# Kernel tuning notes

Hardware: AMD Instinct MI355X
Metric: run time of the kernel (lower is better)

## Reference

```python
import jax, jax.numpy as jnp
import numpy as np

N = 8192      # num voxels (queries)
M = 8192      # num important conv coords (keys)
B = 2         # batch size
MAXZ, MAXY, MAXX = 41, 1440, 1440
PTS, PDIM = 5, 4
PRUNE_RATIO = 0.5
NEG = -1e9


def setup_inputs() -> dict:
    key = jax.random.key(0)
    k = jax.random.split(key, 8)
    bidx = jax.random.randint(k[0], (N, 1), 0, B)
    zyx = jnp.concatenate([
        jax.random.randint(k[1], (N, 1), 0, MAXZ),
        jax.random.randint(k[2], (N, 1), 0, MAXY),
        jax.random.randint(k[3], (N, 1), 0, MAXX)], axis=1)
    voxel_coords = jnp.concatenate([bidx, zyx], axis=1).astype(jnp.int32)  # [N,4] (b,z,y,x)
    kb = jax.random.randint(k[4], (M, 1), 0, B).astype(jnp.float32)
    kc = jax.random.uniform(k[5], (M, 3), dtype=jnp.float32) * jnp.array([MAXZ, MAXY, MAXX], jnp.float32)
    important_conv_coords = jnp.concatenate([kb, kc], axis=1)  # [M,4] float
    voxels = jax.random.normal(k[6], (N, PTS, PDIM), dtype=jnp.float32)
    kw = jax.random.split(k[7], 2)
    w1 = jax.random.normal(kw[0], (3, 32), dtype=jnp.float32) * 0.5
    b1 = jnp.zeros((32,), jnp.float32)
    w2 = jax.random.normal(kw[1], (32, 1), dtype=jnp.float32) * 0.2
    b2 = jnp.zeros((1,), jnp.float32)
    return {"voxel_coords": voxel_coords, "important_conv_coords": important_conv_coords,
            "voxels": voxels, "w1": w1, "b1": b1, "w2": w2, "b2": b2}


def reference(voxel_coords, important_conv_coords, voxels, w1, b1, w2, b2):
    # --- attn_prune_unimportant: per-batch coord attention, vectorized with a batch mask ---
    q = voxel_coords[:, 1:].astype(jnp.float32)           # [N,3]
    qb = voxel_coords[:, 0]                               # [N] batch idx
    keys = important_conv_coords[:, 1:]                   # [M,3]
    kbat = important_conv_coords[:, 0].astype(jnp.int32)  # [M]
    scores = jnp.einsum('nd,md->nm', q, keys) / jnp.sqrt(jnp.float32(3.0))  # [N,M]
    mask = qb[:, None] == kbat[None, :]
    scores = jnp.where(mask, scores, NEG)
    attn = jax.nn.softmax(scores, axis=-1)                # per-batch softmax (masked)
    coords_weight = jnp.einsum('nm,md->nd', attn, keys)   # [N,3]  (values == keys)
    # importance_conv: Linear(3,32) -> ReLU -> Linear(32,1) -> Sigmoid
    h = jax.nn.relu(coords_weight @ w1 + b1)
    importance = jax.nn.sigmoid(h @ w2 + b2)              # [N,1]
    # --- sort-based pruning: drop the lowest-importance fraction ---
    order = jnp.argsort(importance[:, 0])                 # ascending, like torch .sort()
    keep = order[int(N * PRUNE_RATIO):]                   # [K] static size
    important_coords = voxel_coords[keep]                 # [K,4]
    important_voxels = voxels[keep]                       # [K,PTS,PDIM]
    kept_importance = importance[keep]                    # [K,1]
    return important_coords, important_voxels, kept_importance, importance
```

## Files before the change

kernel.cpp:

```cpp
#include <hip/hip_runtime.h>
#include <math.h>

#define NQ   8192
#define MK   8192
#define KEEP 4096

#define OFF_CMAX   0
#define OFF_PART   262144
#define OFF_K64    1310720


typedef unsigned long long ull;

__global__ __launch_bounds__(1024) void attn_kernel(
    const int4*   __restrict__ vcoords,
    const float4* __restrict__ kcoords,
    float* __restrict__ ws)
{
    __shared__ __align__(16) char smem[65792];
    float4* sk   = (float4*)smem;
    float*  red1 = (float*)(smem + 16384);
    float*  red2 = (float*)(smem + 16384 + 16448);
    float4* pf   = (float4*)smem;

    float*  cmaxg = (float*)((char*)ws + OFF_CMAX);
    float4* partg = (float4*)((char*)ws + OFF_PART);

    const int b = blockIdx.x;
    const int g = b >> 3, c = b & 7;
    const int gs = g * 256, cs = c * 1024;
    const int t = threadIdx.x, w = t >> 6, lane = t & 63;

    const int4 v0 = vcoords[gs + lane];
    const int4 v1 = vcoords[gs + lane + 64];
    const int4 v2 = vcoords[gs + lane + 128];
    const int4 v3 = vcoords[gs + lane + 192];
    const float qb0 = (float)v0.x, qz0 = (float)v0.y, qy0 = (float)v0.z, qx0 = (float)v0.w;
    const float qb1 = (float)v1.x, qz1 = (float)v1.y, qy1 = (float)v1.z, qx1 = (float)v1.w;
    const float qb2 = (float)v2.x, qz2 = (float)v2.y, qy2 = (float)v2.z, qx2 = (float)v2.w;
    const float qb3 = (float)v3.x, qz3 = (float)v3.y, qy3 = (float)v3.z, qx3 = (float)v3.w;
    const float is3 = 0.57735026918962576f;

    if (t < 1024) sk[t] = kcoords[cs + t];
    __syncthreads();

    const int jb = w * 64, je = jb + 64;

    float m0 = -INFINITY, m1 = -INFINITY, m2 = -INFINITY, m3 = -INFINITY;
    #pragma unroll 4
    for (int j = jb; j < je; ++j) {
        float4 k4 = sk[j];
        float d0 = fmaf(qz0, k4.y, fmaf(qy0, k4.z, qx0 * k4.w));
        float d1 = fmaf(qz1, k4.y, fmaf(qy1, k4.z, qx1 * k4.w));
        float d2 = fmaf(qz2, k4.y, fmaf(qy2, k4.z, qx2 * k4.w));
        float d3 = fmaf(qz3, k4.y, fmaf(qy3, k4.z, qx3 * k4.w));
        m0 = fmaxf(m0, fmaf(fabsf(k4.x - qb0), -1e10f, d0));
        m1 = fmaxf(m1, fmaf(fabsf(k4.x - qb1), -1e10f, d1));
        m2 = fmaxf(m2, fmaf(fabsf(k4.x - qb2), -1e10f, d2));
        m3 = fmaxf(m3, fmaf(fabsf(k4.x - qb3), -1e10f, d3));
    }
    red1[w * 257 + lane]       = m0;
    red1[w * 257 + lane + 64]  = m1;
    red1[w * 257 + lane + 128] = m2;
    red1[w * 257 + lane + 192] = m3;
    __syncthreads();
    {
        const int col = t >> 2, r4 = (t & 3) * 4;
        float mv = red1[r4 * 257 + col];
        mv = fmaxf(mv, red1[(r4 + 1) * 257 + col]);
        mv = fmaxf(mv, red1[(r4 + 2) * 257 + col]);
        mv = fmaxf(mv, red1[(r4 + 3) * 257 + col]);
        mv = fmaxf(mv, __shfl_xor(mv, 1));
        mv = fmaxf(mv, __shfl_xor(mv, 2));
        if ((t & 3) == 0) {
            red2[col] = mv;
            cmaxg[b * 256 + col] = mv;
        }
    }
    __syncthreads();
    const float mg0 = red2[lane],       cut0 = mg0 - 155.8845727f;
    const float mg1 = red2[lane + 64],  cut1 = mg1 - 155.8845727f;
    const float mg2 = red2[lane + 128], cut2 = mg2 - 155.8845727f;
    const float mg3 = red2[lane + 192], cut3 = mg3 - 155.8845727f;

    float l0 = 0.f, sz0 = 0.f, sy0 = 0.f, sx0 = 0.f;
    float l1 = 0.f, sz1 = 0.f, sy1 = 0.f, sx1 = 0.f;
    float l2 = 0.f, sz2 = 0.f, sy2 = 0.f, sx2 = 0.f;
    float l3 = 0.f, sz3 = 0.f, sy3 = 0.f, sx3 = 0.f;
    #pragma unroll 2
    for (int j = jb; j < je; ++j) {
        float4 k4 = sk[j];
        float d0 = fmaf(qz0, k4.y, fmaf(qy0, k4.z, qx0 * k4.w));
        float d1 = fmaf(qz1, k4.y, fmaf(qy1, k4.z, qx1 * k4.w));
        float d2 = fmaf(qz2, k4.y, fmaf(qy2, k4.z, qx2 * k4.w));
        float d3 = fmaf(qz3, k4.y, fmaf(qy3, k4.z, qx3 * k4.w));
        d0 = fmaf(fabsf(k4.x - qb0), -1e10f, d0);
        d1 = fmaf(fabsf(k4.x - qb1), -1e10f, d1);
        d2 = fmaf(fabsf(k4.x - qb2), -1e10f, d2);
        d3 = fmaf(fabsf(k4.x - qb3), -1e10f, d3);
        bool t0 = d0 >= cut0, t1 = d1 >= cut1, t2 = d2 >= cut2, t3 = d3 >= cut3;
        if (__any(t0 || t1 || t2 || t3)) {
            float e0 = t0 ? expf((d0 - mg0) * is3) : 0.f;
            float e1 = t1 ? expf((d1 - mg1) * is3) : 0.f;
            float e2 = t2 ? expf((d2 - mg2) * is3) : 0.f;
            float e3 = t3 ? expf((d3 - mg3) * is3) : 0.f;
            l0 += e0; sz0 = fmaf(e0, k4.y, sz0); sy0 = fmaf(e0, k4.z, sy0); sx0 = fmaf(e0, k4.w, sx0);
            l1 += e1; sz1 = fmaf(e1, k4.y, sz1); sy1 = fmaf(e1, k4.z, sy1); sx1 = fmaf(e1, k4.w, sx1);
            l2 += e2; sz2 = fmaf(e2, k4.y, sz2); sy2 = fmaf(e2, k4.z, sy2); sx2 = fmaf(e2, k4.w, sx2);
            l3 += e3; sz3 = fmaf(e3, k4.y, sz3); sy3 = fmaf(e3, k4.z, sy3); sx3 = fmaf(e3, k4.w, sx3);
        }
    }
    __syncthreads();
    pf[w * 257 + lane]       = make_float4(l0, sz0, sy0, sx0);
    pf[w * 257 + lane + 64]  = make_float4(l1, sz1, sy1, sx1);
    pf[w * 257 + lane + 128] = make_float4(l2, sz2, sy2, sx2);
    pf[w * 257 + lane + 192] = make_float4(l3, sz3, sy3, sx3);
    __syncthreads();
    {
        const int col = t >> 2, r4 = (t & 3) * 4;
        float4 a = pf[r4 * 257 + col];
        #pragma unroll
        for (int rr = 1; rr < 4; ++rr) {
            float4 p = pf[(r4 + rr) * 257 + col];
            a.x += p.x; a.y += p.y; a.z += p.z; a.w += p.w;
        }
        a.x += __shfl_xor(a.x, 1); a.y += __shfl_xor(a.y, 1);
        a.z += __shfl_xor(a.z, 1); a.w += __shfl_xor(a.w, 1);
        a.x += __shfl_xor(a.x, 2); a.y += __shfl_xor(a.y, 2);
        a.z += __shfl_xor(a.z, 2); a.w += __shfl_xor(a.w, 2);
        if ((t & 3) == 0) partg[b * 256 + col] = a;
    }
}

__global__ __launch_bounds__(256) void mlp_kernel(
    const float* __restrict__ ws,
    const float* __restrict__ w1, const float* __restrict__ b1,
    const float* __restrict__ w2, const float* __restrict__ b2,
    float* __restrict__ out_imp, ull* __restrict__ K64)
{
    const int s = blockIdx.x * 256 + threadIdx.x;
    const int g = s >> 8, q = s & 255;
    const float*  cmaxg = (const float*)((const char*)ws + OFF_CMAX);
    const float4* partg = (const float4*)((const char*)ws + OFF_PART);
    const float is3 = 0.57735026918962576f;

    float cc[8];
    float C = -INFINITY;
    #pragma unroll
    for (int c = 0; c < 8; ++c) {
        cc[c] = cmaxg[(g * 8 + c) * 256 + q];
        C = fmaxf(C, cc[c]);
    }
    float L = 0.f, SZ = 0.f, SY = 0.f, SX = 0.f;
    #pragma unroll
    for (int c = 0; c < 8; ++c) {
        float sc = expf((cc[c] - C) * is3);
        float4 p = partg[(g * 8 + c) * 256 + q];
        L  = fmaf(p.x, sc, L);
        SZ = fmaf(p.y, sc, SZ);
        SY = fmaf(p.z, sc, SY);
        SX = fmaf(p.w, sc, SX);
    }
    float inv = (L > 0.f) ? 1.f / L : 0.f;
    float cz = SZ * inv, cy = SY * inv, cx = SX * inv;
    float logit = b2[0];
    #pragma unroll
    for (int k = 0; k < 32; ++k) {
        float h = b1[k] + cz * w1[k] + cy * w1[32 + k] + cx * w1[64 + k];
        h = fmaxf(h, 0.f);
        logit += h * w2[k];
    }
    float p = 1.f / (1.f + expf(-logit));
    out_imp[s] = p;
    K64[s] = ((ull)__float_as_uint(p) << 32) | (unsigned)s;
}

__global__ __launch_bounds__(1024) void rank_scatter_kernel(
    const ull* __restrict__ K,
    const int4* __restrict__ vcoords,
    const float* __restrict__ voxels,
    float* __restrict__ out)
{
    __shared__ int scnt[16][32];
    __shared__ int rks[32];
    const int t = threadIdx.x, w = t >> 6, lane = t & 63;
    const int ib = blockIdx.x * 32;

    const ull kiv = K[ib + (lane & 31)];
    const int kilo = (int)(unsigned)kiv, kihi = (int)(unsigned)(kiv >> 32);

    const int jb = w * 512;
    ull kj[8];
    #pragma unroll
    for (int r = 0; r < 8; ++r) kj[r] = K[jb + r * 64 + lane];

    int acc = 0;
    for (int i = 0; i < 32; ++i) {
        unsigned lo = (unsigned)__builtin_amdgcn_readlane(kilo, i);
        unsigned hi = (unsigned)__builtin_amdgcn_readlane(kihi, i);
        ull ki = ((ull)hi << 32) | lo;
        int c = 0;
        #pragma unroll
        for (int r = 0; r < 8; ++r)
            c += (int)__popcll(__ballot(kj[r] < ki));
        acc += (lane == i) ? c : 0;
    }
    if (lane < 32) scnt[w][lane] = acc;
    __syncthreads();
    if (t < 32) {
        int rank = 0;
        #pragma unroll
        for (int ww = 0; ww < 16; ++ww) rank += scnt[ww][t];
        rks[t] = rank;
    }
    __syncthreads();

    const int il = t >> 5, r = t & 31;
    const int rank = rks[il];
    if (rank >= KEEP) {
        const int p = rank - KEEP;
        const int i = ib + il;
        if (r < 20) {
            out[16384 + p * 20 + r] = voxels[i * 20 + r];
        } else if (r < 24) {
            const int* vc = (const int*)&vcoords[i];
            out[p * 4 + (r - 20)] = (float)vc[r - 20];
        } else if (r == 24) {
            out[98304 + p] = __uint_as_float((unsigned)(K[i] >> 32));
        }
    }
}

extern "C" void kernel_launch(void* const* d_in, const int* in_sizes, int n_in,
                              void* d_out, int out_size, void* d_ws, size_t ws_size,
                              hipStream_t stream) {
    const int4*   vcoords = (const int4*)d_in[0];
    const float4* kcoords = (const float4*)d_in[1];
    const float*  voxels  = (const float*)d_in[2];
    const float*  w1      = (const float*)d_in[3];
    const float*  b1      = (const float*)d_in[4];
    const float*  w2      = (const float*)d_in[5];
    const float*  b2      = (const float*)d_in[6];
    float* out = (float*)d_out;
    float* ws  = (float*)d_ws;
    ull* K64   = (ull*)((char*)d_ws + OFF_K64);

    attn_kernel<<<256, 1024, 0, stream>>>(vcoords, kcoords, ws);
    mlp_kernel<<<32, 256, 0, stream>>>(ws, w1, b1, w2, b2, out + 102400, K64);
    rank_scatter_kernel<<<256, 1024, 0, stream>>>(K64, vcoords, voxels, out);
}
```

Before: 104.4 us.

## Partition keys by batch in shared memory and split attention loops per batch

Keys loaded into shared memory are compacted with a ballot/popcount prefix so batch-0 keys come first and batch-1 keys follow. Each wave then runs separate loops over the batch-0 and batch-1 key ranges, so the per-key batch mask arithmetic (fabs/fma penalty) is dropped and queries choose the matching max or cutoff. Queries still evaluate both ranges but only accumulate for their own batch, and a guard is added in the combine step for chunks with no matching keys (max of -inf). This assumes batch ids are only 0 or 1, and it adds a block sync plus some loop-splitting overhead.

```diff
diff --git a/kernel.cpp b/kernel.cpp
--- a/kernel.cpp
+++ b/kernel.cpp
@@ -21,6 +21,7 @@
     float4* sk   = (float4*)smem;
     float*  red1 = (float*)(smem + 16384);
     float*  red2 = (float*)(smem + 16384 + 16448);
+    int*    wc   = (int*)(smem + 33856);
     float4* pf   = (float4*)smem;
 
     float*  cmaxg = (float*)((char*)ws + OFF_CMAX);
@@ -35,34 +36,54 @@
     const int4 v1 = vcoords[gs + lane + 64];
     const int4 v2 = vcoords[gs + lane + 128];
     const int4 v3 = vcoords[gs + lane + 192];
-    const float qb0 = (float)v0.x, qz0 = (float)v0.y, qy0 = (float)v0.z, qx0 = (float)v0.w;
-    const float qb1 = (float)v1.x, qz1 = (float)v1.y, qy1 = (float)v1.z, qx1 = (float)v1.w;
-    const float qb2 = (float)v2.x, qz2 = (float)v2.y, qy2 = (float)v2.z, qx2 = (float)v2.w;
-    const float qb3 = (float)v3.x, qz3 = (float)v3.y, qy3 = (float)v3.z, qx3 = (float)v3.w;
+    const float qz0 = (float)v0.y, qy0 = (float)v0.z, qx0 = (float)v0.w;
+    const float qz1 = (float)v1.y, qy1 = (float)v1.z, qx1 = (float)v1.w;
+    const float qz2 = (float)v2.y, qy2 = (float)v2.z, qx2 = (float)v2.w;
+    const float qz3 = (float)v3.y, qy3 = (float)v3.z, qx3 = (float)v3.w;
+    const bool qb0 = (v0.x != 0), qb1 = (v1.x != 0);
+    const bool qb2 = (v2.x != 0), qb3 = (v3.x != 0);
     const float is3 = 0.57735026918962576f;
 
-    if (t < 1024) sk[t] = kcoords[cs + t];
+    float4 k4s = kcoords[cs + t];
+    ull bal = __ballot(k4s.x == 0.0f);
+    if (lane == 0) wc[w] = (int)__popcll(bal);
+    __syncthreads();
+    int woff = 0, n0 = 0;
+    #pragma unroll
+    for (int i = 0; i < 16; ++i) { int cv = wc[i]; n0 += cv; if (i < w) woff += cv; }
+    {
+        int bef = (int)__popcll(bal & ((1ull << lane) - 1));
+        int dst = (k4s.x == 0.0f) ? (woff + bef) : (n0 + t - woff - bef);
+        sk[dst] = k4s;
+    }
     __syncthreads();
 
     const int jb = w * 64, je = jb + 64;
-
-    float m0 = -INFINITY, m1 = -INFINITY, m2 = -INFINITY, m3 = -INFINITY;
+    const int jeA = min(je, n0);
+    const int jbB = max(jb, n0);
+
+    float mA0 = -INFINITY, mA1 = -INFINITY, mA2 = -INFINITY, mA3 = -INFINITY;
+    float mB0 = -INFINITY, mB1 = -INFINITY, mB2 = -INFINITY, mB3 = -INFINITY;
     #pragma unroll 4
-    for (int j = jb; j < je; ++j) {
-        float4 k4 = sk[j];
-        float d0 = fmaf(qz0, k4.y, fmaf(qy0, k4.z, qx0 * k4.w));
-        float d1 = fmaf(qz1, k4.y, fmaf(qy1, k4.z, qx1 * k4.w));
-        float d2 = fmaf(qz2, k4.y, fmaf(qy2, k4.z, qx2 * k4.w));
-        float d3 = fmaf(qz3, k4.y, fmaf(qy3, k4.z, qx3 * k4.w));
-        m0 = fmaxf(m0, fmaf(fabsf(k4.x - qb0), -1e10f, d0));
-        m1 = fmaxf(m1, fmaf(fabsf(k4.x - qb1), -1e10f, d1));
-        m2 = fmaxf(m2, fmaf(fabsf(k4.x - qb2), -1e10f, d2));
-        m3 = fmaxf(m3, fmaf(fabsf(k4.x - qb3), -1e10f, d3));
-    }
-    red1[w * 257 + lane]       = m0;
-    red1[w * 257 + lane + 64]  = m1;
-    red1[w * 257 + lane + 128] = m2;
-    red1[w * 257 + lane + 192] = m3;
+    for (int j = jb; j < jeA; ++j) {
+        float4 k4 = sk[j];
+        mA0 = fmaxf(mA0, fmaf(qz0, k4.y, fmaf(qy0, k4.z, qx0 * k4.w)));
+        mA1 = fmaxf(mA1, fmaf(qz1, k4.y, fmaf(qy1, k4.z, qx1 * k4.w)));
+        mA2 = fmaxf(mA2, fmaf(qz2, k4.y, fmaf(qy2, k4.z, qx2 * k4.w)));
+        mA3 = fmaxf(mA3, fmaf(qz3, k4.y, fmaf(qy3, k4.z, qx3 * k4.w)));
+    }
+    #pragma unroll 4
+    for (int j = jbB; j < je; ++j) {
+        float4 k4 = sk[j];
+        mB0 = fmaxf(mB0, fmaf(qz0, k4.y, fmaf(qy0, k4.z, qx0 * k4.w)));
+        mB1 = fmaxf(mB1, fmaf(qz1, k4.y, fmaf(qy1, k4.z, qx1 * k4.w)));
+        mB2 = fmaxf(mB2, fmaf(qz2, k4.y, fmaf(qy2, k4.z, qx2 * k4.w)));
+        mB3 = fmaxf(mB3, fmaf(qz3, k4.y, fmaf(qy3, k4.z, qx3 * k4.w)));
+    }
+    red1[w * 257 + lane]       = qb0 ? mB0 : mA0;
+    red1[w * 257 + lane + 64]  = qb1 ? mB1 : mA1;
+    red1[w * 257 + lane + 128] = qb2 ? mB2 : mA2;
+    red1[w * 257 + lane + 192] = qb3 ? mB3 : mA3;
     __syncthreads();
     {
         const int col = t >> 2, r4 = (t & 3) * 4;
@@ -82,23 +103,42 @@
     const float mg1 = red2[lane + 64],  cut1 = mg1 - 155.8845727f;
     const float mg2 = red2[lane + 128], cut2 = mg2 - 155.8845727f;
     const float mg3 = red2[lane + 192], cut3 = mg3 - 155.8845727f;
+    const float cA0 = qb0 ? INFINITY : cut0, cB0 = qb0 ? cut0 : INFINITY;
+    const float cA1 = qb1 ? INFINITY : cut1, cB1 = qb1 ? cut1 : INFINITY;
+    const float cA2 = qb2 ? INFINITY : cut2, cB2 = qb2 ? cut2 : INFINITY;
+    const float cA3 = qb3 ? INFINITY : cut3, cB3 = qb3 ? cut3 : INFINITY;
 
     float l0 = 0.f, sz0 = 0.f, sy0 = 0.f, sx0 = 0.f;
     float l1 = 0.f, sz1 = 0.f, sy1 = 0.f, sx1 = 0.f;
     float l2 = 0.f, sz2 = 0.f, sy2 = 0.f, sx2 = 0.f;
     float l3 = 0.f, sz3 = 0.f, sy3 = 0.f, sx3 = 0.f;
     #pragma unroll 2
-    for (int j = jb; j < je; ++j) {
+    for (int j = jb; j < jeA; ++j) {
         float4 k4 = sk[j];
         float d0 = fmaf(qz0, k4.y, fmaf(qy0, k4.z, qx0 * k4.w));
         float d1 = fmaf(qz1, k4.y, fmaf(qy1, k4.z, qx1 * k4.w));
         float d2 = fmaf(qz2, k4.y, fmaf(qy2, k4.z, qx2 * k4.w));
         float d3 = fmaf(qz3, k4.y, fmaf(qy3, k4.z, qx3 * k4.w));
-        d0 = fmaf(fabsf(k4.x - qb0), -1e10f, d0);
-        d1 = fmaf(fabsf(k4.x - qb1), -1e10f, d1);
-        d2 = fmaf(fabsf(k4.x - qb2), -1e10f, d2);
-        d3 = fmaf(fabsf(k4.x - qb3), -1e10f, d3);
-        bool t0 = d0 >= cut0, t1 = d1 >= cut1, t2 = d2 >= cut2, t3 = d3 >= cut3;
+        bool t0 = d0 >= cA0, t1 = d1 >= cA1, t2 = d2 >= cA2, t3 = d3 >= cA3;
+        if (__any(t0 || t1 || t2 || t3)) {
+            float e0 = t0 ? expf((d0 - mg0) * is3) : 0.f;
+            float e1 = t1 ? expf((d1 - mg1) * is3) : 0.f;
+            float e2 = t2 ? expf((d2 - mg2) * is3) : 0.f;
+            float e3 = t3 ? expf((d3 - mg3) * is3) : 0.f;
+            l0 += e0; sz0 = fmaf(e0, k4.y, sz0); sy0 = fmaf(e0, k4.z, sy0); sx0 = fmaf(e0, k4.w, sx0);
+            l1 += e1; sz1 = fmaf(e1, k4.y, sz1); sy1 = fmaf(e1, k4.z, sy1); sx1 = fmaf(e1, k4.w, sx1);
+            l2 += e2; sz2 = fmaf(e2, k4.y, sz2); sy2 = fmaf(e2, k4.z, sy2); sx2 = fmaf(e2, k4.w, sx2);
+            l3 += e3; sz3 = fmaf(e3, k4.y, sz3); sy3 = fmaf(e3, k4.z, sy3); sx3 = fmaf(e3, k4.w, sx3);
+        }
+    }
+    #pragma unroll 2
+    for (int j = jbB; j < je; ++j) {
+        float4 k4 = sk[j];
+        float d0 = fmaf(qz0, k4.y, fmaf(qy0, k4.z, qx0 * k4.w));
+        float d1 = fmaf(qz1, k4.y, fmaf(qy1, k4.z, qx1 * k4.w));
+        float d2 = fmaf(qz2, k4.y, fmaf(qy2, k4.z, qx2 * k4.w));
+        float d3 = fmaf(qz3, k4.y, fmaf(qy3, k4.z, qx3 * k4.w));
+        bool t0 = d0 >= cB0, t1 = d1 >= cB1, t2 = d2 >= cB2, t3 = d3 >= cB3;
         if (__any(t0 || t1 || t2 || t3)) {
             float e0 = t0 ? expf((d0 - mg0) * is3) : 0.f;
             float e1 = t1 ? expf((d1 - mg1) * is3) : 0.f;
@@ -154,7 +194,7 @@
     float L = 0.f, SZ = 0.f, SY = 0.f, SX = 0.f;
     #pragma unroll
     for (int c = 0; c < 8; ++c) {
-        float sc = expf((cc[c] - C) * is3);
+        float sc = (cc[c] == -INFINITY) ? 0.f : expf((cc[c] - C) * is3);
         float4 p = partg[(g * 8 + c) * 256 + q];
         L  = fmaf(p.x, sc, L);
         SZ = fmaf(p.y, sc, SZ);
@@ -199,11 +239,11 @@
         unsigned lo = (unsigned)__builtin_amdgcn_readlane(kilo, i);
         unsigned hi = (unsigned)__builtin_amdgcn_readlane(kihi, i);
         ull ki = ((ull)hi << 32) | lo;
-        int c = 0;
+        int cc = 0;
         #pragma unroll
         for (int r = 0; r < 8; ++r)
-            c += (int)__popcll(__ballot(kj[r] < ki));
-        acc += (lane == i) ? c : 0;
+            cc += (int)__popcll(__ballot(kj[r] < ki));
+        acc += (lane == i) ? cc : 0;
     }
     if (lane < 32) scnt[w][lane] = acc;
     __syncthreads();
```

Measured after the change: 112.4 us. 7.6% more time.
